# Kernel optimization log

Hardware: AMD Instinct MI355X
Metric: run time of the kernel (lower is better)

## Reference

```python
import jax, jax.numpy as jnp
import numpy as np

EPS = 1e-8
ALPHA, BETA, DELTA = 0.3, 0.4, 0.1  # gamma branch (EAGT) disabled: use_eagt=0 -> zeros
RANK_LR, ROLE_DIM, ROLE_ITERS, ROLE_LR = 8, 8, 80, 0.05
SPEC_RANK, SPEC_MOM, SPEC_TAU = 16, 4, 1.0
CAND_K, SPARSE_K = 20, 20


def _norm_score(s):
    # safe_normalize_score: standardize
    return (s - s.mean()) / (s.std() + EPS)


def _norm_sq(A):
    # normalize_square_matrix(fill_diag=0, abs_value=True)
    n = A.shape[0]
    A = jnp.abs(A) * (1.0 - jnp.eye(n, dtype=A.dtype))
    return A / (A.max() + EPS)


def _masked_row_softmax(A):
    mask = A != 0
    sm = jax.nn.softmax(jnp.where(mask, A, -jnp.inf), axis=-1)
    return jnp.where(mask, sm, 0.0)


def _topk_row(A, k):
    vals, idx = jax.lax.top_k(A, k)
    rows = jnp.arange(A.shape[0])[:, None]
    return jnp.zeros_like(A).at[rows, idx].set(vals)


def _sym_nmf(M, rank, iters, lr):
    # symmetric NMF: min ||M - W W^T||^2, GD with nonnegativity clamp, eig-based init
    vals, vecs = jnp.linalg.eigh(0.5 * (M + M.T))
    W0 = jnp.abs(vecs[:, -rank:]) * jnp.sqrt(jnp.abs(vals[-rank:]))[None, :]  # [N,r]
    def step(W, _):
        G = 4.0 * ((W @ W.T - M) @ W)
        return jnp.maximum(W - lr * G, 0.0), None
    W, _ = jax.lax.scan(step, W0, None, length=iters)
    return W


def _spec_sig(M):
    # normalized top-eigenvalue moments -> [SPEC_MOM]
    ev = jnp.linalg.eigvalsh(0.5 * (M + M.T))
    top = jax.lax.top_k(jnp.abs(ev), SPEC_RANK)[0]
    top = top / (top[0] + EPS)
    return jnp.stack([(top ** (m + 1)).mean() for m in range(SPEC_MOM)])


def _forward(x_target, A_original, src_signatures, src_role_B, mlp_w1, mlp_b1, mlp_w2, mlp_b2):
    B, N, T, C = x_target.shape
    s = x_target.mean(axis=(0, 3))                       # [N,T] node series
    mu, sd = s.mean(1), s.std(1)
    sn = (s - mu[:, None]) / (sd[:, None] + EPS)
    c0 = sn @ sn.T / T                                   # lag-0 correlation [N,N]
    cl = sn[:, :-1] @ sn[:, 1:].T / (T - 1)              # lag-1 correlation (directed)
    R = 0.5 * (jnp.abs(c0) + jnp.abs(0.5 * (cl + cl.T)))  # corr_lagcorr relation matrix

    # candidate edges: per-row topk, exclude self loops -> pairs [E=N*K, 2]
    _, idx = jax.lax.top_k(R - 1e9 * jnp.eye(N, dtype=R.dtype), CAND_K)
    rows = jnp.repeat(jnp.arange(N), CAND_K)
    cols = idx.reshape(-1)

    M0 = jax.lax.stop_gradient(R)                        # build_relation_matrix under no_grad

    # low-rank branch (no_grad)
    U, S, Vh = jnp.linalg.svd(M0, full_matrices=False)
    L = (U[:, :RANK_LR] * S[:RANK_LR]) @ Vh[:RANK_LR]
    A_lr = _masked_row_softmax(_norm_sq(L))
    score_lr = A_lr[rows, cols]

    # spectral-signature source weights rho (no_grad)
    sig_t = _spec_sig(M0)
    dist = ((src_signatures - sig_t[None, :]) ** 2).sum(-1)
    rho = jax.nn.softmax(-dist / SPEC_TAU)               # [M]

    # iterative symmetric NMF roles + fused source role matrix (no_grad)
    W_t = _sym_nmf(M0, ROLE_DIM, ROLE_ITERS, ROLE_LR)    # [N,r]
    Beff = jnp.einsum('m,mrs->rs', rho, src_role_B)      # sum_m rho_m B_m
    A_role = _norm_sq(W_t @ Beff @ W_t.T)
    score_role = A_role[rows, cols]

    # residual MLP branch (differentiable): [E,8] edge features
    dots = s @ s.T
    nrm = jnp.sqrt((s * s).sum(1))
    cosm = dots / (nrm[:, None] * nrm[None, :] + EPS)
    feats = jnp.stack([c0[rows, cols], cl[rows, cols], cl[cols, rows], cosm[rows, cols],
                       mu[rows], mu[cols], sd[rows], sd[cols]], axis=-1)
    h = jax.nn.relu(feats @ mlp_w1 + mlp_b1)
    score_res = (h @ mlp_w2 + mlp_b2)[:, 0]

    score_final = (ALPHA * _norm_score(jax.lax.stop_gradient(score_lr))
                   + BETA * _norm_score(jax.lax.stop_gradient(score_role))
                   + DELTA * _norm_score(score_res))

    A = jnp.zeros((N, N), x_target.dtype).at[rows, cols].set(jax.nn.sigmoid(score_final))
    A = _topk_row(_masked_row_softmax(A), SPARSE_K)
    # _match_original_batch: A_original is [B,N,N] -> expand
    return jnp.broadcast_to(A[None], A_original.shape)


def setup_inputs():
    key = jax.random.key(0)
    ks = jax.random.split(key, 6)
    B, N, T, C, Msrc = 16, 1024, 96, 2, 3
    return {
        'x_target': jax.random.normal(ks[0], (B, N, T, C), jnp.float32),
        'A_original': jax.random.uniform(ks[1], (B, N, N), jnp.float32),
        'src_signatures': jax.random.uniform(ks[2], (Msrc, SPEC_MOM), jnp.float32),
        'src_role_B': jax.random.uniform(ks[3], (Msrc, ROLE_DIM, ROLE_DIM), jnp.float32),
        'mlp_w1': jax.random.normal(ks[4], (8, 32), jnp.float32) * 0.3,
        'mlp_b1': jnp.zeros((32,), jnp.float32),
        'mlp_w2': jax.random.normal(ks[5], (32, 1), jnp.float32) * 0.3,
        'mlp_b2': jnp.zeros((1,), jnp.float32),
    }


def reference(x_target, A_original, src_signatures, src_role_B, mlp_w1, mlp_b1, mlp_w2, mlp_b2):
    return _forward(x_target, A_original, src_signatures, src_role_B, mlp_w1, mlp_b1, mlp_w2, mlp_b2)
```

## Files before the change

kernel.cpp:

```cpp
#include <hip/hip_runtime.h>
#include <stdint.h>

#define N_ 1024
#define T_ 96
#define KRY 96
#define EDG 20480
#define EPS 1e-8f
#define GRID 64

enum : size_t {
  O_SN   = 0,
  O_S    = O_SN + (size_t)N_*T_,
  O_MU   = O_S + (size_t)N_*T_,
  O_SD   = O_MU + N_,
  O_NRM  = O_SD + N_,
  O_C0   = O_NRM + N_,
  O_CL   = O_C0 + (size_t)N_*N_,
  O_R    = O_CL + (size_t)N_*N_,
  O_AL   = O_R  + (size_t)N_*N_,
  O_AP   = O_AL + (size_t)N_*N_,
  O_V    = O_AP + (size_t)N_*N_,
  O_YA   = O_V + (size_t)KRY*N_,
  O_ALP  = O_YA + N_,
  O_BET  = O_ALP + 128,
  O_EV   = O_BET + 128,
  O_YS   = O_EV + 128,
  O_LS   = O_YS + 16*KRY,
  O_BEFF = O_LS + 16,
  O_SCAL = O_BEFF + 64,
  O_BARL = O_SCAL + 64,
  O_BARN = O_BARL + 384,
  O_NSLOT= O_BARN + 384,
  O_DOT0 = O_NSLOT + 64,
  O_DOT1 = O_DOT0 + (size_t)KRY*GRID,
  O_RML  = O_DOT1 + (size_t)KRY*GRID,
  O_RDL  = O_RML + N_,
  O_RMP  = O_RDL + N_,
  O_RDP  = O_RMP + N_,
  O_UM   = O_RDP + N_,
  O_WA   = O_UM + (size_t)N_*8,
  O_WB   = O_WA + (size_t)N_*8,
  O_SLR  = O_WB + (size_t)N_*8,
  O_SRO  = O_SLR + EDG,
  O_SRE  = O_SRO + EDG,
  O_IDX  = O_SRE + EDG,
  O_END  = O_IDX + EDG
};

__device__ __forceinline__ float hashf(unsigned x){
  x ^= x >> 16; x *= 0x7feb352dU; x ^= x >> 15; x *= 0x846ca68bU; x ^= x >> 16;
  return (float)(x & 0xFFFFFFu) * (1.f/16777216.f) - 0.5f;
}

#define BSTR 32
__device__ __forceinline__ void gbar(unsigned* bar){
  __syncthreads();
  if (threadIdx.x == 0){
    __builtin_amdgcn_fence(__ATOMIC_RELEASE, "agent");
    unsigned g = __hip_atomic_load(&bar[9*BSTR], __ATOMIC_RELAXED, __HIP_MEMORY_SCOPE_AGENT);
    unsigned leaf = (blockIdx.x & 7u)*BSTR;
    unsigned lv = __hip_atomic_fetch_add(&bar[leaf], 1u, __ATOMIC_RELAXED, __HIP_MEMORY_SCOPE_AGENT) + 1u;
    if (lv == (g+1u)*8u){
      unsigned rv = __hip_atomic_fetch_add(&bar[8*BSTR], 1u, __ATOMIC_RELAXED, __HIP_MEMORY_SCOPE_AGENT) + 1u;
      if (rv == (g+1u)*8u)
        __hip_atomic_store(&bar[9*BSTR], g+1u, __ATOMIC_RELAXED, __HIP_MEMORY_SCOPE_AGENT);
    }
    while (__hip_atomic_load(&bar[9*BSTR], __ATOMIC_RELAXED, __HIP_MEMORY_SCOPE_AGENT) == g)
      __builtin_amdgcn_s_sleep(2);
    __builtin_amdgcn_fence(__ATOMIC_ACQUIRE, "agent");
  }
  __syncthreads();
}

__global__ void kInit(float* ws){
  int t = threadIdx.x;
  if (t < 896) ws[O_SCAL + t] = 0.f;
}

__global__ __launch_bounds__(256) void kSeries(const float* x, float* ws){
  __shared__ float sm[192];
  __shared__ float red[256];
  int n = blockIdx.x, tid = threadIdx.x;
  if (tid < 192){
    float acc = 0.f;
    size_t base = (size_t)n*192 + tid;
    for (int b = 0; b < 16; ++b) acc += x[base + (size_t)b*196608];
    sm[tid] = acc;
  }
  __syncthreads();
  float sval = 0.f;
  if (tid < 96) sval = (sm[2*tid] + sm[2*tid+1]) * (1.f/32.f);
  red[tid] = (tid < 96) ? sval : 0.f; __syncthreads();
  for (int s = 128; s > 0; s >>= 1){ if (tid < s) red[tid] += red[tid+s]; __syncthreads(); }
  float mu = red[0] * (1.f/96.f); __syncthreads();
  red[tid] = (tid < 96) ? sval*sval : 0.f; __syncthreads();
  for (int s = 128; s > 0; s >>= 1){ if (tid < s) red[tid] += red[tid+s]; __syncthreads(); }
  float nrm = sqrtf(red[0]); __syncthreads();
  float dev = sval - mu;
  red[tid] = (tid < 96) ? dev*dev : 0.f; __syncthreads();
  for (int s = 128; s > 0; s >>= 1){ if (tid < s) red[tid] += red[tid+s]; __syncthreads(); }
  float sd = sqrtf(red[0] * (1.f/96.f));
  if (tid < 96){
    ws[O_S  + (size_t)n*96 + tid] = sval;
    ws[O_SN + (size_t)n*96 + tid] = dev / (sd + EPS);
  }
  if (tid == 0){ ws[O_MU+n] = mu; ws[O_SD+n] = sd; ws[O_NRM+n] = nrm; }
}

__global__ __launch_bounds__(256) void kCorr(float* ws){
  __shared__ float A[16][97], B[16][97];
  int bi = blockIdx.x, bj = blockIdx.y, tid = threadIdx.x;
  for (int l = tid; l < 16*96; l += 256){
    int r = l / 96, t = l % 96;
    A[r][t] = ws[O_SN + (size_t)(bi*16+r)*96 + t];
    B[r][t] = ws[O_SN + (size_t)(bj*16+r)*96 + t];
  }
  __syncthreads();
  int ti = tid >> 4, tj = tid & 15;
  int i = bi*16 + ti, j = bj*16 + tj;
  float c0 = 0.f, cl = 0.f;
  for (int t = 0; t < 96; ++t) c0 += A[ti][t]*B[tj][t];
  for (int t = 0; t < 95; ++t) cl += A[ti][t]*B[tj][t+1];
  ws[O_C0 + (size_t)i*N_ + j] = c0 * (1.f/96.f);
  ws[O_CL + (size_t)i*N_ + j] = cl * (1.f/95.f);
}

__global__ __launch_bounds__(256) void kR(float* ws){
  __shared__ float tl[32][33];
  int bi = blockIdx.x, bj = blockIdx.y, tid = threadIdx.x;
  for (int l = tid; l < 1024; l += 256){
    int r = l >> 5, c = l & 31;
    tl[r][c] = ws[O_CL + (size_t)(bj*32+r)*N_ + bi*32 + c];
  }
  __syncthreads();
  for (int l = tid; l < 1024; l += 256){
    int il = l >> 5, jl = l & 31;
    int i = bi*32 + il, j = bj*32 + jl;
    float c0 = ws[O_C0 + (size_t)i*N_ + j];
    float cl = ws[O_CL + (size_t)i*N_ + j];
    float clt = tl[jl][il];
    ws[O_R + (size_t)i*N_ + j] = 0.5f*(fabsf(c0) + fabsf(0.5f*(cl + clt)));
  }
}

__global__ __launch_bounds__(256) void kTopK(float* ws){
  __shared__ float v[1024];
  __shared__ float rv[256];
  __shared__ int ri[256];
  int r = blockIdx.x, tid = threadIdx.x;
  for (int l = tid; l < 1024; l += 256) v[l] = ws[O_R + (size_t)r*N_ + l];
  __syncthreads();
  if (tid == 0) v[r] = -3.4e38f;
  __syncthreads();
  int* idx = (int*)(ws + O_IDX);
  for (int t = 0; t < 20; ++t){
    float best = -3.4e38f; int bi = 1 << 30;
    for (int l = tid; l < 1024; l += 256){
      float vv = v[l];
      if (vv > best || (vv == best && l < bi)){ best = vv; bi = l; }
    }
    rv[tid] = best; ri[tid] = bi; __syncthreads();
    for (int s = 128; s > 0; s >>= 1){
      if (tid < s){
        if (rv[tid+s] > rv[tid] || (rv[tid+s] == rv[tid] && ri[tid+s] < ri[tid])){
          rv[tid] = rv[tid+s]; ri[tid] = ri[tid+s];
        }
      }
      __syncthreads();
    }
    if (tid == 0){ idx[r*20 + t] = ri[0]; v[ri[0]] = -3.4e38f; }
    __syncthreads();
  }
}

__global__ __launch_bounds__(256) void kLanczos(float* ws){
  unsigned* bar = (unsigned*)(ws + O_BARL);
  __shared__ float vsh[1024];
  __shared__ float red[272];
  __shared__ float yls[16];
  __shared__ float csh[KRY];
  const int b = blockIdx.x, tid = threadIdx.x;
  const int i0 = b*16;
  float* slots = ws + O_NSLOT;
  float* dot0  = ws + O_DOT0;
  float* dot1  = ws + O_DOT1;
  float* y     = ws + O_YA;

  {
    float ss = 0.f;
    if (tid < 16){
      float v = hashf((unsigned)(i0 + tid + 12345));
      y[i0 + tid] = v;
      ss = v*v;
    }
    red[tid] = ss; __syncthreads();
    for (int s = 128; s > 0; s >>= 1){ if (tid < s) red[tid] += red[tid+s]; __syncthreads(); }
    if (tid == 0) slots[b] = red[0];
  }
  gbar(bar);

  for (int k = 0; k < KRY; ++k){
    {
      float t = (tid < GRID) ? slots[tid] : 0.f;
      red[tid] = t; __syncthreads();
      for (int s = 128; s > 0; s >>= 1){ if (tid < s) red[tid] += red[tid+s]; __syncthreads(); }
      float inv = rsqrtf(fmaxf(red[0], 1e-30f));
      __syncthreads();
      for (int l = tid; l < 1024; l += 256) vsh[l] = y[l]*inv;
      __syncthreads();
      if (tid < 16) ws[O_V + (size_t)k*N_ + i0 + tid] = vsh[i0 + tid];
      int wave = tid >> 6, lane = tid & 63;
      for (int rr = 0; rr < 4; ++rr){
        int r = i0 + wave*4 + rr;
        const float* row = ws + O_R + (size_t)r*N_;
        float acc = 0.f;
        for (int t2 = lane; t2 < 1024; t2 += 64) acc += row[t2]*vsh[t2];
        for (int off = 32; off > 0; off >>= 1) acc += __shfl_down(acc, off, 64);
        if (lane == 0) yls[wave*4 + rr] = acc;
      }
      __syncthreads();
      if (tid <= k){
        const float* vj = ws + O_V + (size_t)tid*N_ + i0;
        float acc = 0.f;
        #pragma unroll
        for (int q = 0; q < 16; ++q) acc += vj[q]*yls[q];
        dot0[tid*GRID + b] = acc;
      }
    }
    gbar(bar);
    {
      if (tid <= k){
        const float* pr = dot0 + (size_t)tid*GRID;
        float acc = 0.f;
        #pragma unroll
        for (int q = 0; q < GRID; ++q) acc += pr[q];
        csh[tid] = acc;
        if (b == 0){
          if (tid == k)   ws[O_ALP + k] = acc;
          if (tid == k-1) ws[O_BET + k] = acc;
        }
      }
      __syncthreads();
      if (k == KRY-1) break;
      int il = tid & 15, chunk = tid >> 4;
      float part = 0.f;
      for (int j = chunk; j <= k; j += 16) part += csh[j]*ws[O_V + (size_t)j*N_ + i0 + il];
      red[il*17 + chunk] = part;
      __syncthreads();
      if (tid < 16){
        float corr = 0.f;
        #pragma unroll
        for (int q = 0; q < 16; ++q) corr += red[tid*17 + q];
        yls[tid] -= corr;
      }
      __syncthreads();
      if (tid <= k){
        const float* vj = ws + O_V + (size_t)tid*N_ + i0;
        float acc = 0.f;
        #pragma unroll
        for (int q = 0; q < 16; ++q) acc += vj[q]*yls[q];
        dot1[tid*GRID + b] = acc;
      }
    }
    gbar(bar);
    {
      if (tid <= k){
        const float* pr = dot1 + (size_t)tid*GRID;
        float acc = 0.f;
        #pragma unroll
        for (int q = 0; q < GRID; ++q) acc += pr[q];
        csh[tid] = acc;
      }
      __syncthreads();
      int il = tid & 15, chunk = tid >> 4;
      float part = 0.f;
      for (int j = chunk; j <= k; j += 16) part += csh[j]*ws[O_V + (size_t)j*N_ + i0 + il];
      red[il*17 + chunk] = part;
      __syncthreads();
      if (tid < 16){
        float corr = 0.f;
        #pragma unroll
        for (int q = 0; q < 16; ++q) corr += red[tid*17 + q];
        float nv = yls[tid] - corr;
        yls[tid] = nv;
        y[i0 + tid] = nv;
        red[tid*17 + 16] = nv*nv;
      }
      __syncthreads();
      if (tid == 0){
        float ss = 0.f;
        #pragma unroll
        for (int q = 0; q < 16; ++q) ss += red[q*17 + 16];
        slots[b] = ss;
      }
    }
    gbar(bar);
  }
}

__global__ __launch_bounds__(256) void kEigen(float* ws, const float* srcsig, const float* srcB){
  __shared__ float a[KRY], bt[KRY], b2[KRY], ev[KRY];
  __shared__ float Dw[16][KRY], U1w[16][KRY], U2w[16][KRY], Xw[16][KRY];
  __shared__ int slotidx[16];
  __shared__ float slam[16];
  __shared__ float glo_s, ghi_s;
  int tid = threadIdx.x;
  if (tid < KRY){
    a[tid] = ws[O_ALP + tid];
    float b = (tid >= 1) ? ws[O_BET + tid] : 0.f;
    bt[tid] = b; b2[tid] = b*b;
  }
  __syncthreads();
  if (tid == 0){
    float lo = 3.4e38f, hi = -3.4e38f;
    for (int i = 0; i < KRY; ++i){
      float r = fabsf(bt[i]) + ((i < KRY-1) ? fabsf(bt[i+1]) : 0.f);
      lo = fminf(lo, a[i] - r); hi = fmaxf(hi, a[i] + r);
    }
    glo_s = lo - 1.f; ghi_s = hi + 1.f;
  }
  __syncthreads();
  if (tid < KRY){
    float lo = glo_s, hi = ghi_s;
    for (int it = 0; it < 60; ++it){
      float mid = 0.5f*(lo + hi);
      int cnt = 0; float d = 1.f;
      for (int kk = 0; kk < KRY; ++kk){
        d = (a[kk] - mid) - ((kk > 0) ? b2[kk]/d : 0.f);
        if (d < 0.f) cnt++;
        if (fabsf(d) < 1e-20f) d = -1e-20f;
      }
      if (cnt <= tid) lo = mid; else hi = mid;
    }
    ev[tid] = 0.5f*(lo + hi);
    ws[O_EV + tid] = ev[tid];
  }
  __syncthreads();
  if (tid == 0){
    int hiI = KRY-1, loI = 0;
    float topv[16]; int magidx[16];
    for (int t = 0; t < 16; ++t){
      if (fabsf(ev[hiI]) >= fabsf(ev[loI])) magidx[t] = hiI--;
      else magidx[t] = loI++;
      topv[t] = fabsf(ev[magidx[t]]);
    }
    for (int s = 0; s < 8; ++s){ slotidx[s] = magidx[s]; slam[s] = ev[magidx[s]]; }
    for (int s = 0; s < 8; ++s){ slotidx[8+s] = KRY-8 + s; slam[8+s] = ev[KRY-8+s]; }
    float t0 = topv[0] + EPS;
    float sig[4];
    for (int m = 0; m < 4; ++m){
      float acc = 0.f;
      for (int t = 0; t < 16; ++t){
        float x = topv[t]/t0, p = x;
        for (int q = 0; q < m; ++q) p *= x;
        acc += p;
      }
      sig[m] = acc * (1.f/16.f);
    }
    float dist[3];
    for (int m = 0; m < 3; ++m){
      float acc = 0.f;
      for (int kq = 0; kq < 4; ++kq){ float dd = srcsig[m*4+kq] - sig[kq]; acc += dd*dd; }
      dist[m] = acc;
    }
    float mx = fmaxf(fmaxf(-dist[0], -dist[1]), -dist[2]);
    float e0 = expf(-dist[0]-mx), e1 = expf(-dist[1]-mx), e2 = expf(-dist[2]-mx);
    float sinv = 1.f/(e0+e1+e2);
    float rho0 = e0*sinv, rho1 = e1*sinv, rho2 = e2*sinv;
    for (int rr = 0; rr < 8; ++rr)
      for (int ss = 0; ss < 8; ++ss)
        ws[O_BEFF + rr*8 + ss] = rho0*srcB[rr*8+ss] + rho1*srcB[64+rr*8+ss] + rho2*srcB[128+rr*8+ss];
    for (int s = 0; s < 16; ++s) ws[O_LS + s] = slam[s];
  }
  __syncthreads();
  if (tid < 16){
    int s = tid, ei = slotidx[s];
    float lam = ev[ei];
    for (int pass = 0; pass < 2; ++pass){
      for (int i = 0; i < KRY; ++i){
        Dw[s][i] = a[i] - lam;
        U1w[s][i] = (i < KRY-1) ? bt[i+1] : 0.f;
        U2w[s][i] = 0.f;
        if (pass == 0) Xw[s][i] = hashf((unsigned)(ei*1024 + i + 777));
      }
      for (int i = 0; i < KRY-1; ++i){
        float p1 = Dw[s][i], q1 = U1w[s][i], r1 = U2w[s][i], x1 = Xw[s][i];
        float p2 = bt[i+1], q2 = Dw[s][i+1], rr2 = U1w[s][i+1], x2 = Xw[s][i+1];
        if (fabsf(p2) > fabsf(p1)){
          float t;
          t=p1;p1=p2;p2=t; t=q1;q1=q2;q2=t; t=r1;r1=rr2;rr2=t; t=x1;x1=x2;x2=t;
        }
        if (fabsf(p1) < 1e-20f) p1 = (p1 < 0.f) ? -1e-20f : 1e-20f;
        float m = p2/p1;
        Dw[s][i]=p1; U1w[s][i]=q1; U2w[s][i]=r1; Xw[s][i]=x1;
        Dw[s][i+1] = q2 - m*q1; U1w[s][i+1] = rr2 - m*r1; Xw[s][i+1] = x2 - m*x1;
      }
      {
        float dd = Dw[s][KRY-1]; if (fabsf(dd) < 1e-20f) dd = 1e-20f;
        Xw[s][KRY-1] = Xw[s][KRY-1]/dd;
      }
      {
        float dd = Dw[s][KRY-2]; if (fabsf(dd) < 1e-20f) dd = 1e-20f;
        Xw[s][KRY-2] = (Xw[s][KRY-2] - U1w[s][KRY-2]*Xw[s][KRY-1])/dd;
      }
      for (int i = KRY-3; i >= 0; --i){
        float dd = Dw[s][i]; if (fabsf(dd) < 1e-20f) dd = 1e-20f;
        Xw[s][i] = (Xw[s][i] - U1w[s][i]*Xw[s][i+1] - U2w[s][i]*Xw[s][i+2])/dd;
      }
      float nn = 0.f;
      for (int i = 0; i < KRY; ++i) nn += Xw[s][i]*Xw[s][i];
      float inv = rsqrtf(fmaxf(nn, 1e-37f));
      for (int i = 0; i < KRY; ++i) Xw[s][i] *= inv;
    }
  }
  __syncthreads();
  if (tid == 0){
    for (int s = 1; s < 16; ++s)
      for (int t = 0; t < s; ++t){
        if (slotidx[t] == slotidx[s]) continue;
        if (fabsf(slam[t] - slam[s]) > 1e-2f) continue;
        float dp = 0.f;
        for (int i = 0; i < KRY; ++i) dp += Xw[s][i]*Xw[t][i];
        for (int i = 0; i < KRY; ++i) Xw[s][i] -= dp*Xw[t][i];
        float nn = 0.f;
        for (int i = 0; i < KRY; ++i) nn += Xw[s][i]*Xw[s][i];
        float inv = rsqrtf(fmaxf(nn, 1e-37f));
        for (int i = 0; i < KRY; ++i) Xw[s][i] *= inv;
      }
  }
  __syncthreads();
  for (int l = tid; l < 16*KRY; l += 256) ws[O_YS + l] = Xw[l/KRY][l%KRY];
}

__global__ __launch_bounds__(256) void kRitz(float* ws){
  __shared__ float ysh[16][KRY];
  __shared__ float lam[16];
  int tid = threadIdx.x;
  for (int l = tid; l < 16*KRY; l += 256) ysh[l/KRY][l%KRY] = ws[O_YS + l];
  if (tid < 16) lam[tid] = ws[O_LS + tid];
  __syncthreads();
  int i = blockIdx.x*256 + tid;
  float acc[16];
  #pragma unroll
  for (int s = 0; s < 16; ++s) acc[s] = 0.f;
  for (int k = 0; k < KRY; ++k){
    float v = ws[O_V + (size_t)k*N_ + i];
    #pragma unroll
    for (int s = 0; s < 16; ++s) acc[s] += v*ysh[s][k];
  }
  #pragma unroll
  for (int s = 0; s < 8; ++s) ws[O_UM + (size_t)i*8 + s] = acc[s];
  #pragma unroll
  for (int c = 0; c < 8; ++c) ws[O_WA + (size_t)i*8 + c] = sqrtf(fabsf(lam[8+c]))*fabsf(acc[8+c]);
}

__global__ __launch_bounds__(256) void kL(float* ws){
  __shared__ float Ua[32][8], Ub[32][8], lam[8];
  __shared__ float red[256];
  int bi = blockIdx.x, bj = blockIdx.y, tid = threadIdx.x;
  if (tid < 8) lam[tid] = ws[O_LS + tid];
  int r = tid >> 3, c = tid & 7;
  Ua[r][c] = ws[O_UM + (size_t)(bi*32+r)*8 + c];
  Ub[r][c] = ws[O_UM + (size_t)(bj*32+r)*8 + c];
  __syncthreads();
  float bmax = 0.f;
  for (int l = tid; l < 1024; l += 256){
    int il = l >> 5, jl = l & 31;
    int i = bi*32 + il, j = bj*32 + jl;
    float acc = 0.f;
    #pragma unroll
    for (int q = 0; q < 8; ++q) acc += lam[q]*Ua[il][q]*Ub[jl][q];
    float v = fabsf(acc);
    if (i == j) v = 0.f;
    ws[O_AL + (size_t)i*N_ + j] = v;
    bmax = fmaxf(bmax, v);
  }
  red[tid] = bmax; __syncthreads();
  for (int s = 128; s > 0; s >>= 1){ if (tid < s) red[tid] = fmaxf(red[tid], red[tid+s]); __syncthreads(); }
  if (tid == 0) atomicMax((int*)(ws + O_SCAL + 0), __float_as_int(red[0]));
}

__global__ __launch_bounds__(256) void kRowStats(float* ws, int which){
  __shared__ float red[256];
  size_t src = which ? O_AP : O_AL;
  float mxall = __int_as_float(((int*)(ws + O_SCAL))[which]);
  float d = 1.f/(mxall + EPS);
  int r = blockIdx.x, tid = threadIdx.x;
  const float* row = ws + src + (size_t)r*N_;
  float m = 0.f;
  for (int l = tid; l < 1024; l += 256) m = fmaxf(m, row[l]);
  red[tid] = m; __syncthreads();
  for (int s = 128; s > 0; s >>= 1){ if (tid < s) red[tid] = fmaxf(red[tid], red[tid+s]); __syncthreads(); }
  float rmax = red[0]*d; __syncthreads();
  float acc = 0.f;
  for (int l = tid; l < 1024; l += 256){ float v = row[l]; if (v != 0.f) acc += expf(v*d - rmax); }
  red[tid] = acc; __syncthreads();
  for (int s = 128; s > 0; s >>= 1){ if (tid < s) red[tid] += red[tid+s]; __syncthreads(); }
  if (tid == 0){
    ws[(which ? O_RMP : O_RML) + r] = rmax;
    ws[(which ? O_RDP : O_RDL) + r] = red[0];
  }
}

__global__ __launch_bounds__(256) void kNmf(float* ws){
  unsigned* bar = (unsigned*)(ws + O_BARN);
  __shared__ float Wl[1024][8];
  __shared__ float G[64];
  __shared__ float red2[256];
  int b = blockIdx.x, tid = threadIdx.x;
  int r0 = b*16;
  for (int it = 0; it < 80; ++it){
    const float* Win = ws + ((it & 1) ? O_WB : O_WA);
    float* Wout      = ws + ((it & 1) ? O_WA : O_WB);
    for (int l = tid; l < 8192; l += 256) Wl[l >> 3][l & 7] = Win[l];
    __syncthreads();
    {
      int p = tid >> 2, q = tid & 3;
      int rr = p >> 3, cc = p & 7;
      float acc = 0.f;
      for (int t = q*256; t < q*256 + 256; ++t) acc += Wl[t][rr]*Wl[t][cc];
      red2[tid] = acc; __syncthreads();
      if (q == 0) G[p] = red2[tid] + red2[tid+1] + red2[tid+2] + red2[tid+3];
      __syncthreads();
    }
    {
      int half = tid & 1;
      int pr = tid >> 1;
      int lr = pr >> 3, j = pr & 7;
      int grow = r0 + lr;
      const float* rrow = ws + O_R + (size_t)grow*N_;
      float acc = 0.f;
      for (int t = half*512; t < half*512 + 512; ++t) acc += rrow[t]*Wl[t][j];
      red2[tid] = acc; __syncthreads();
      if (half == 0){
        float rw = red2[tid] + red2[tid+1];
        float wg = 0.f;
        #pragma unroll
        for (int c = 0; c < 8; ++c) wg += Wl[grow][c]*G[c*8 + j];
        float val = Wl[grow][j] - 0.2f*(wg - rw);
        Wout[(size_t)grow*8 + j] = fmaxf(val, 0.f);
      }
      __syncthreads();
    }
    gbar(bar);
  }
}

__global__ __launch_bounds__(256) void kP(float* ws){
  __shared__ float B[64];
  __shared__ float Wa[8][32], Wb2[8][32];
  __shared__ float red[256];
  int bi = blockIdx.x, bj = blockIdx.y, tid = threadIdx.x;
  if (tid < 64) B[tid] = ws[O_BEFF + tid];
  __syncthreads();
  {
    int c = tid >> 5, il = tid & 31;
    Wb2[c][il] = ws[O_WA + (size_t)(bj*32+il)*8 + c];
  }
  __syncthreads();
  {
    int r = tid >> 5, il = tid & 31;
    float acc = 0.f;
    #pragma unroll
    for (int c = 0; c < 8; ++c) acc += ws[O_WA + (size_t)(bi*32+il)*8 + c]*B[c*8 + r];
    Wa[r][il] = acc;
  }
  __syncthreads();
  float bmax = 0.f;
  for (int l = tid; l < 1024; l += 256){
    int il = l >> 5, jl = l & 31;
    int i = bi*32+il, j = bj*32+jl;
    float acc = 0.f;
    #pragma unroll
    for (int q = 0; q < 8; ++q) acc += Wa[q][il]*Wb2[q][jl];
    float v = fabsf(acc);
    if (i == j) v = 0.f;
    ws[O_AP + (size_t)i*N_ + j] = v;
    bmax = fmaxf(bmax, v);
  }
  red[tid] = bmax; __syncthreads();
  for (int s = 128; s > 0; s >>= 1){ if (tid < s) red[tid] = fmaxf(red[tid], red[tid+s]); __syncthreads(); }
  if (tid == 0) atomicMax((int*)(ws + O_SCAL + 1), __float_as_int(red[0]));
}

__global__ __launch_bounds__(256) void kEdges(float* ws, const float* w1, const float* b1,
                                              const float* w2, const float* b2){
  __shared__ float W1[256], B1[32], W2[32], B2;
  int tid = threadIdx.x;
  if (tid < 256) W1[tid] = w1[tid];
  if (tid < 32){ B1[tid] = b1[tid]; W2[tid] = w2[tid]; }
  if (tid == 0) B2 = b2[0];
  __syncthreads();
  int e = blockIdx.x*256 + tid;
  if (e >= EDG) return;
  int r = e/20;
  int c = ((const int*)(ws + O_IDX))[e];
  float dL = 1.f/(__int_as_float(((int*)(ws+O_SCAL))[0]) + EPS);
  float aL = ws[O_AL + (size_t)r*N_ + c];
  float slr = 0.f;
  if (aL != 0.f){ float den = ws[O_RDL + r]; if (den > 0.f) slr = expf(aL*dL - ws[O_RML + r])/den; }
  float dP = 1.f/(__int_as_float(((int*)(ws+O_SCAL))[1]) + EPS);
  float aP = ws[O_AP + (size_t)r*N_ + c];
  float sro = 0.f;
  if (aP != 0.f){ float den = ws[O_RDP + r]; if (den > 0.f) sro = expf(aP*dP - ws[O_RMP + r])/den; }
  float dots = 0.f;
  const float* srow = ws + O_S + (size_t)r*T_;
  const float* scol = ws + O_S + (size_t)c*T_;
  for (int t = 0; t < 96; ++t) dots += srow[t]*scol[t];
  float cosm = dots/(ws[O_NRM+r]*ws[O_NRM+c] + EPS);
  float f[8];
  f[0] = ws[O_C0 + (size_t)r*N_ + c];
  f[1] = ws[O_CL + (size_t)r*N_ + c];
  f[2] = ws[O_CL + (size_t)c*N_ + r];
  f[3] = cosm;
  f[4] = ws[O_MU + r]; f[5] = ws[O_MU + c];
  f[6] = ws[O_SD + r]; f[7] = ws[O_SD + c];
  float sres = B2;
  for (int jj = 0; jj < 32; ++jj){
    float h = B1[jj];
    #pragma unroll
    for (int q = 0; q < 8; ++q) h += f[q]*W1[q*32 + jj];
    h = fmaxf(h, 0.f);
    sres += h*W2[jj];
  }
  ws[O_SLR + e] = slr; ws[O_SRO + e] = sro; ws[O_SRE + e] = sres;
}

__global__ __launch_bounds__(1024) void kStats(float* ws){
  __shared__ float red[1024];
  int tid = threadIdx.x;
  for (int arr = 0; arr < 3; ++arr){
    const float* x = (arr == 0) ? ws + O_SLR : ((arr == 1) ? ws + O_SRO : ws + O_SRE);
    float acc = 0.f;
    for (int l = tid; l < EDG; l += 1024) acc += x[l];
    red[tid] = acc; __syncthreads();
    for (int s = 512; s > 0; s >>= 1){ if (tid < s) red[tid] += red[tid+s]; __syncthreads(); }
    float mean = red[0]/(float)EDG; __syncthreads();
    float acc2 = 0.f;
    for (int l = tid; l < EDG; l += 1024){ float d = x[l]-mean; acc2 += d*d; }
    red[tid] = acc2; __syncthreads();
    for (int s = 512; s > 0; s >>= 1){ if (tid < s) red[tid] += red[tid+s]; __syncthreads(); }
    if (tid == 0){
      float var = red[0]/(float)EDG;
      ws[O_SCAL + 2 + arr*2] = mean;
      ws[O_SCAL + 3 + arr*2] = 1.f/(sqrtf(var) + EPS);
    }
    __syncthreads();
  }
}

__global__ __launch_bounds__(256) void kOut(float* ws, float* out){
  __shared__ __align__(16) float row[1024];
  __shared__ float sv[20];
  __shared__ int cols[20];
  int r = blockIdx.x, tid = threadIdx.x;
  for (int l = tid; l < 1024; l += 256) row[l] = 0.f;
  if (tid < 20){
    int e = r*20 + tid;
    float m1 = ws[O_SCAL+2], k1 = ws[O_SCAL+3];
    float m2 = ws[O_SCAL+4], k2 = ws[O_SCAL+5];
    float m3 = ws[O_SCAL+6], k3 = ws[O_SCAL+7];
    float v = 0.3f*(ws[O_SLR+e]-m1)*k1 + 0.4f*(ws[O_SRO+e]-m2)*k2 + 0.1f*(ws[O_SRE+e]-m3)*k3;
    sv[tid] = 1.f/(1.f + expf(-v));
    cols[tid] = ((const int*)(ws + O_IDX))[e];
  }
  __syncthreads();
  if (tid == 0){
    float mx = sv[0];
    for (int q = 1; q < 20; ++q) mx = fmaxf(mx, sv[q]);
    float den = 0.f; float ex[20];
    for (int q = 0; q < 20; ++q){ ex[q] = expf(sv[q]-mx); den += ex[q]; }
    float inv = 1.f/den;
    for (int q = 0; q < 20; ++q) row[cols[q]] = ex[q]*inv;
  }
  __syncthreads();
  const float4* r4 = (const float4*)row;
  for (int b = 0; b < 16; ++b){
    float4* dst = (float4*)(out + (size_t)b*1048576 + (size_t)r*1024);
    dst[tid] = r4[tid];
  }
}

extern "C" void kernel_launch(void* const* d_in, const int* in_sizes, int n_in,
                              void* d_out, int out_size, void* d_ws, size_t ws_size,
                              hipStream_t stream) {
  (void)in_sizes; (void)n_in; (void)out_size; (void)ws_size;
  const float* x   = (const float*)d_in[0];
  const float* sig = (const float*)d_in[2];
  const float* rB  = (const float*)d_in[3];
  const float* w1  = (const float*)d_in[4];
  const float* b1  = (const float*)d_in[5];
  const float* w2  = (const float*)d_in[6];
  const float* b2  = (const float*)d_in[7];
  float* w = (float*)d_ws;
  float* out = (float*)d_out;

  kInit<<<1, 1024, 0, stream>>>(w);
  kSeries<<<1024, 256, 0, stream>>>(x, w);
  kCorr<<<dim3(64,64), 256, 0, stream>>>(w);
  kR<<<dim3(32,32), 256, 0, stream>>>(w);
  kTopK<<<1024, 256, 0, stream>>>(w);

  kLanczos<<<GRID, 256, 0, stream>>>(w);
  kEigen<<<1, 256, 0, stream>>>(w, sig, rB);
  kRitz<<<4, 256, 0, stream>>>(w);

  kL<<<dim3(32,32), 256, 0, stream>>>(w);
  kRowStats<<<1024, 256, 0, stream>>>(w, 0);

  kNmf<<<GRID, 256, 0, stream>>>(w);
  kP<<<dim3(32,32), 256, 0, stream>>>(w);
  kRowStats<<<1024, 256, 0, stream>>>(w, 1);

  kEdges<<<80, 256, 0, stream>>>(w, w1, b1, w2, b2);
  kStats<<<1, 1024, 0, stream>>>(w);
  kOut<<<1024, 256, 0, stream>>>(w, out);
}
```

Measured before the change: 4.514 ms.

## Fuse top-k into Lanczos launch, simplify grid barrier, vectorize loads

The per-row top-k kernel now runs as extra blocks in the same launch as the Lanczos solver, so it can overlap with the 64 persistent Lanczos blocks instead of running serially before them. The grid barrier becomes a monotonic counter with a caller-supplied epoch, which removes the generation read and the second-level store, and the NMF loop skips its final barrier. The Lanczos matvec handles four rows per wave in one pass, the norm reduction uses wave shuffles, partial-dot buffers are laid out per block, and the y/W loads use float4. The risk is that the persistent barrier assumes all 64 Lanczos blocks are co-resident while 1024 extra top-k blocks compete for slots, and the barrier counters are assumed to start at zero.

```diff
diff --git a/kernel.cpp b/kernel.cpp
--- a/kernel.cpp
+++ b/kernel.cpp
@@ -32,8 +32,8 @@
   O_BARN = O_BARL + 384,
   O_NSLOT= O_BARN + 384,
   O_DOT0 = O_NSLOT + 64,
-  O_DOT1 = O_DOT0 + (size_t)KRY*GRID,
-  O_RML  = O_DOT1 + (size_t)KRY*GRID,
+  O_DOT1 = O_DOT0 + (size_t)GRID*128,
+  O_RML  = O_DOT1 + (size_t)GRID*128,
   O_RDL  = O_RML + N_,
   O_RMP  = O_RDL + N_,
   O_RDP  = O_RMP + N_,
@@ -53,20 +53,16 @@
 }
 
 #define BSTR 32
-__device__ __forceinline__ void gbar(unsigned* bar){
+__device__ __forceinline__ void gbar(unsigned* bar, unsigned n){
   __syncthreads();
   if (threadIdx.x == 0){
     __builtin_amdgcn_fence(__ATOMIC_RELEASE, "agent");
-    unsigned g = __hip_atomic_load(&bar[9*BSTR], __ATOMIC_RELAXED, __HIP_MEMORY_SCOPE_AGENT);
     unsigned leaf = (blockIdx.x & 7u)*BSTR;
     unsigned lv = __hip_atomic_fetch_add(&bar[leaf], 1u, __ATOMIC_RELAXED, __HIP_MEMORY_SCOPE_AGENT) + 1u;
-    if (lv == (g+1u)*8u){
-      unsigned rv = __hip_atomic_fetch_add(&bar[8*BSTR], 1u, __ATOMIC_RELAXED, __HIP_MEMORY_SCOPE_AGENT) + 1u;
-      if (rv == (g+1u)*8u)
-        __hip_atomic_store(&bar[9*BSTR], g+1u, __ATOMIC_RELAXED, __HIP_MEMORY_SCOPE_AGENT);
-    }
-    while (__hip_atomic_load(&bar[9*BSTR], __ATOMIC_RELAXED, __HIP_MEMORY_SCOPE_AGENT) == g)
-      __builtin_amdgcn_s_sleep(2);
+    if (lv == n*8u)
+      __hip_atomic_fetch_add(&bar[8*BSTR], 1u, __ATOMIC_RELAXED, __HIP_MEMORY_SCOPE_AGENT);
+    while (__hip_atomic_load(&bar[8*BSTR], __ATOMIC_RELAXED, __HIP_MEMORY_SCOPE_AGENT) < n*8u)
+      __builtin_amdgcn_s_sleep(1);
     __builtin_amdgcn_fence(__ATOMIC_ACQUIRE, "agent");
   }
   __syncthreads();
@@ -143,39 +139,40 @@
   }
 }
 
-__global__ __launch_bounds__(256) void kTopK(float* ws){
-  __shared__ float v[1024];
-  __shared__ float rv[256];
-  __shared__ int ri[256];
-  int r = blockIdx.x, tid = threadIdx.x;
-  for (int l = tid; l < 1024; l += 256) v[l] = ws[O_R + (size_t)r*N_ + l];
-  __syncthreads();
-  if (tid == 0) v[r] = -3.4e38f;
-  __syncthreads();
-  int* idx = (int*)(ws + O_IDX);
-  for (int t = 0; t < 20; ++t){
-    float best = -3.4e38f; int bi = 1 << 30;
-    for (int l = tid; l < 1024; l += 256){
-      float vv = v[l];
-      if (vv > best || (vv == best && l < bi)){ best = vv; bi = l; }
-    }
-    rv[tid] = best; ri[tid] = bi; __syncthreads();
-    for (int s = 128; s > 0; s >>= 1){
-      if (tid < s){
-        if (rv[tid+s] > rv[tid] || (rv[tid+s] == rv[tid] && ri[tid+s] < ri[tid])){
-          rv[tid] = rv[tid+s]; ri[tid] = ri[tid+s];
+__global__ __launch_bounds__(256) void kLanczos(float* ws){
+  __shared__ float tv[1024];
+  __shared__ float trv[256];
+  __shared__ int tri[256];
+  if (blockIdx.x >= GRID){
+    int r = blockIdx.x - GRID, tid = threadIdx.x;
+    for (int l = tid; l < 1024; l += 256) tv[l] = ws[O_R + (size_t)r*N_ + l];
+    __syncthreads();
+    if (tid == 0) tv[r] = -3.4e38f;
+    __syncthreads();
+    int* idx = (int*)(ws + O_IDX);
+    for (int t = 0; t < 20; ++t){
+      float best = -3.4e38f; int bi = 1 << 30;
+      for (int l = tid; l < 1024; l += 256){
+        float vv = tv[l];
+        if (vv > best || (vv == best && l < bi)){ best = vv; bi = l; }
+      }
+      trv[tid] = best; tri[tid] = bi; __syncthreads();
+      for (int s = 128; s > 0; s >>= 1){
+        if (tid < s){
+          if (trv[tid+s] > trv[tid] || (trv[tid+s] == trv[tid] && tri[tid+s] < tri[tid])){
+            trv[tid] = trv[tid+s]; tri[tid] = tri[tid+s];
+          }
         }
-      }
-      __syncthreads();
-    }
-    if (tid == 0){ idx[r*20 + t] = ri[0]; v[ri[0]] = -3.4e38f; }
-    __syncthreads();
-  }
-}
-
-__global__ __launch_bounds__(256) void kLanczos(float* ws){
+        __syncthreads();
+      }
+      if (tid == 0){ idx[r*20 + t] = tri[0]; tv[tri[0]] = -3.4e38f; }
+      __syncthreads();
+    }
+    return;
+  }
+
   unsigned* bar = (unsigned*)(ws + O_BARL);
-  __shared__ float vsh[1024];
+  __shared__ __align__(16) float vsh[1024];
   __shared__ float red[272];
   __shared__ float yls[16];
   __shared__ float csh[KRY];
@@ -185,6 +182,7 @@
   float* dot0  = ws + O_DOT0;
   float* dot1  = ws + O_DOT1;
   float* y     = ws + O_YA;
+  unsigned nb = 0;
 
   {
     float ss = 0.f;
@@ -197,26 +195,45 @@
     for (int s = 128; s > 0; s >>= 1){ if (tid < s) red[tid] += red[tid+s]; __syncthreads(); }
     if (tid == 0) slots[b] = red[0];
   }
-  gbar(bar);
+  gbar(bar, ++nb);
 
   for (int k = 0; k < KRY; ++k){
     {
-      float t = (tid < GRID) ? slots[tid] : 0.f;
-      red[tid] = t; __syncthreads();
-      for (int s = 128; s > 0; s >>= 1){ if (tid < s) red[tid] += red[tid+s]; __syncthreads(); }
+      if (tid < 64){
+        float t = slots[tid];
+        for (int off = 32; off > 0; off >>= 1) t += __shfl_down(t, off, 64);
+        if (tid == 0) red[0] = t;
+      }
+      __syncthreads();
       float inv = rsqrtf(fmaxf(red[0], 1e-30f));
-      __syncthreads();
-      for (int l = tid; l < 1024; l += 256) vsh[l] = y[l]*inv;
+      {
+        float4 yv = ((const float4*)y)[tid];
+        float4* vs4 = (float4*)vsh;
+        vs4[tid] = make_float4(yv.x*inv, yv.y*inv, yv.z*inv, yv.w*inv);
+      }
       __syncthreads();
       if (tid < 16) ws[O_V + (size_t)k*N_ + i0 + tid] = vsh[i0 + tid];
       int wave = tid >> 6, lane = tid & 63;
-      for (int rr = 0; rr < 4; ++rr){
-        int r = i0 + wave*4 + rr;
-        const float* row = ws + O_R + (size_t)r*N_;
-        float acc = 0.f;
-        for (int t2 = lane; t2 < 1024; t2 += 64) acc += row[t2]*vsh[t2];
-        for (int off = 32; off > 0; off >>= 1) acc += __shfl_down(acc, off, 64);
-        if (lane == 0) yls[wave*4 + rr] = acc;
+      {
+        const float* r0p = ws + O_R + (size_t)(i0 + wave*4)*N_;
+        float a0 = 0.f, a1 = 0.f, a2 = 0.f, a3 = 0.f;
+        for (int t2 = lane; t2 < 1024; t2 += 64){
+          float vv = vsh[t2];
+          a0 += r0p[t2]*vv;
+          a1 += r0p[N_ + t2]*vv;
+          a2 += r0p[2*N_ + t2]*vv;
+          a3 += r0p[3*N_ + t2]*vv;
+        }
+        for (int off = 32; off > 0; off >>= 1){
+          a0 += __shfl_down(a0, off, 64);
+          a1 += __shfl_down(a1, off, 64);
+          a2 += __shfl_down(a2, off, 64);
+          a3 += __shfl_down(a3, off, 64);
+        }
+        if (lane == 0){
+          yls[wave*4 + 0] = a0; yls[wave*4 + 1] = a1;
+          yls[wave*4 + 2] = a2; yls[wave*4 + 3] = a3;
+        }
       }
       __syncthreads();
       if (tid <= k){
@@ -224,16 +241,15 @@
         float acc = 0.f;
         #pragma unroll
         for (int q = 0; q < 16; ++q) acc += vj[q]*yls[q];
-        dot0[tid*GRID + b] = acc;
-      }
-    }
-    gbar(bar);
+        dot0[(size_t)b*128 + tid] = acc;
+      }
+    }
+    gbar(bar, ++nb);
     {
       if (tid <= k){
-        const float* pr = dot0 + (size_t)tid*GRID;
         float acc = 0.f;
         #pragma unroll
-        for (int q = 0; q < GRID; ++q) acc += pr[q];
+        for (int q = 0; q < GRID; ++q) acc += dot0[(size_t)q*128 + tid];
         csh[tid] = acc;
         if (b == 0){
           if (tid == k)   ws[O_ALP + k] = acc;
@@ -259,16 +275,15 @@
         float acc = 0.f;
         #pragma unroll
         for (int q = 0; q < 16; ++q) acc += vj[q]*yls[q];
-        dot1[tid*GRID + b] = acc;
-      }
-    }
-    gbar(bar);
+        dot1[(size_t)b*128 + tid] = acc;
+      }
+    }
+    gbar(bar, ++nb);
     {
       if (tid <= k){
-        const float* pr = dot1 + (size_t)tid*GRID;
         float acc = 0.f;
         #pragma unroll
-        for (int q = 0; q < GRID; ++q) acc += pr[q];
+        for (int q = 0; q < GRID; ++q) acc += dot1[(size_t)q*128 + tid];
         csh[tid] = acc;
       }
       __syncthreads();
@@ -294,7 +309,7 @@
         slots[b] = ss;
       }
     }
-    gbar(bar);
+    gbar(bar, ++nb);
   }
 }
 
@@ -512,7 +527,14 @@
   for (int it = 0; it < 80; ++it){
     const float* Win = ws + ((it & 1) ? O_WB : O_WA);
     float* Wout      = ws + ((it & 1) ? O_WA : O_WB);
-    for (int l = tid; l < 8192; l += 256) Wl[l >> 3][l & 7] = Win[l];
+    {
+      const float4* W4 = (const float4*)Win;
+      for (int l = tid; l < 2048; l += 256){
+        float4 w = W4[l];
+        int rr = l >> 1, cc = (l & 1)*4;
+        Wl[rr][cc] = w.x; Wl[rr][cc+1] = w.y; Wl[rr][cc+2] = w.z; Wl[rr][cc+3] = w.w;
+      }
+    }
     __syncthreads();
     {
       int p = tid >> 2, q = tid & 3;
@@ -542,7 +564,7 @@
       }
       __syncthreads();
     }
-    gbar(bar);
+    if (it != 79) gbar(bar, (unsigned)(it + 1));
   }
 }
 
@@ -699,9 +721,8 @@
   kSeries<<<1024, 256, 0, stream>>>(x, w);
   kCorr<<<dim3(64,64), 256, 0, stream>>>(w);
   kR<<<dim3(32,32), 256, 0, stream>>>(w);
-  kTopK<<<1024, 256, 0, stream>>>(w);
-
-  kLanczos<<<GRID, 256, 0, stream>>>(w);
+
+  kLanczos<<<GRID + 1024, 256, 0, stream>>>(w);
   kEigen<<<1, 256, 0, stream>>>(w, sig, rB);
   kRitz<<<4, 256, 0, stream>>>(w);
 
```

New measurement: 6.119 ms. 35.6% more time.
